# Kernel tuning notes

Measured on AMD Instinct MI355X. Metric: run time of the kernel, lower is better.

## Reference

```python
import jax, jax.numpy as jnp
import numpy as np

LEVEL = 0.1
SEED = 12345
RAND_MAX = 4294967295.0
BN_EPS = 1e-5


def lcg_noise(n):
    # Original: seed_{t+1} = (65539*seed_t + 1) & 0xFFFFFFFF; value_t = seed_{t+1}/RAND_MAX
    # Closed form: seed_{t+1} = M^{t+1} * s0 + sum_{k=0}^{t} M^k  (mod 2^32).
    # uint32 arithmetic wraps mod 2^32, so cumprod/cumsum give exact jump-ahead.
    m = jnp.full((n,), 65539, dtype=jnp.uint32)
    powers = jnp.cumprod(m)  # M^1 .. M^n (mod 2^32)
    geom = jnp.cumsum(jnp.concatenate([jnp.ones((1,), jnp.uint32), powers[:-1]]))  # sum_{k=0}^{t} M^k
    seeds = powers * jnp.uint32(SEED) + geom  # wraps mod 2^32
    return seeds.astype(jnp.float32) * jnp.float32(LEVEL / RAND_MAX)


def setup_inputs() -> dict:
    key = jax.random.key(0)
    k1, k2 = jax.random.split(key)
    B, Cin, Cout, H, W = 32, 256, 512, 64, 64
    x = jax.random.normal(k1, (B, Cin, H, W), dtype=jnp.float32)
    conv_w = jax.random.normal(k2, (Cout, Cin), dtype=jnp.float32) * 0.02
    conv_b = jnp.zeros((Cout,), dtype=jnp.float32)
    gamma = jnp.ones((Cout,), dtype=jnp.float32)
    beta = jnp.zeros((Cout,), dtype=jnp.float32)
    return {"x": x, "conv_w": conv_w, "conv_b": conv_b, "gamma": gamma, "beta": beta}


def reference(x, conv_w, conv_b, gamma, beta):
    B, C, H, W = x.shape
    noise = lcg_noise(C * H * W).reshape(C, H, W)  # batch-independent, broadcast over B
    x2 = jax.nn.relu(x + noise[None])
    # 1x1 conv == per-pixel GEMM
    y = jnp.einsum('bchw,oc->bohw', x2, conv_w) + conv_b[None, :, None, None]
    # BatchNorm2d (training mode: batch statistics, biased variance)
    mean = jnp.mean(y, axis=(0, 2, 3))
    var = jnp.var(y, axis=(0, 2, 3))
    y_hat = (y - mean[None, :, None, None]) * jax.lax.rsqrt(var + BN_EPS)[None, :, None, None]
    return y_hat * gamma[None, :, None, None] + beta[None, :, None, None]
```

## Files before the change

kernel.cpp:

```cpp
#include <hip/hip_runtime.h>
#include <cstdint>

#define B_    32
#define CIN   256
#define COUT  512
#define HW    4096
#define NPIX  (B_ * HW)
#define NOISE_N (CIN * HW)
#define WN    (COUT * CIN)

typedef _Float16 f16;
typedef _Float16 f16x8 __attribute__((ext_vector_type(8)));
typedef float    f32x4 __attribute__((ext_vector_type(4)));

__device__ __forceinline__ unsigned lcg_seed_after(unsigned n) {
  unsigned A = 1u, Bc = 0u;
  unsigned mA = 65539u, mB = 1u;
  #pragma unroll
  for (int i = 0; i < 21; ++i) {
    if (n & (1u << i)) { A = mA * A; Bc = mA * Bc + mB; }
    mB = mA * mB + mB;
    mA = mA * mA;
  }
  return A * 12345u + Bc;
}

__global__ void k_prep(const float* __restrict__ conv_w,
                       float* __restrict__ noise, f16* __restrict__ w2) {
  const int tid = blockIdx.x * 256 + threadIdx.x;
  if (tid < NOISE_N) {
    const unsigned seed = lcg_seed_after((unsigned)tid + 1u);
    noise[tid] = (float)seed * (float)(0.1 / 4294967295.0);
  } else {
    const int i = tid - NOISE_N;
    if (i < WN) w2[i] = (f16)conv_w[i];
  }
}

__global__ __launch_bounds__(1024) void k1_gram(
    const float* __restrict__ x, const float* __restrict__ noise,
    f16* __restrict__ x2t, float* __restrict__ gpart,
    float* __restrict__ sums, int npart, int useAtomic) {
  __shared__ unsigned char sm[65536];
  const int t = threadIdx.x;
  const int lane = t & 63;
  const int w = t >> 6;
  const int wm = w >> 2, wn = w & 3;
  const int bid = blockIdx.x;
  const int b = bid >> 3;
  const int hw0 = (bid & 7) << 9;

  const int pslot = t & 31;
  const int crow0 = t >> 5;

  f32x4 acc[4][4];
  #pragma unroll
  for (int i = 0; i < 4; ++i)
    #pragma unroll
    for (int j = 0; j < 4; ++j)
      acc[i][j] = (f32x4){0.f, 0.f, 0.f, 0.f};
  float csum[8] = {0.f, 0.f, 0.f, 0.f, 0.f, 0.f, 0.f, 0.f};

  for (int s = 0; s < 4; ++s) {
    const int hwS = hw0 + s * 128;
    #pragma unroll
    for (int cc = 0; cc < 8; ++cc) {
      const int c = crow0 + 32 * cc;
      const float4 xv = *(const float4*)(x + (((size_t)(b * CIN + c)) << 12) + hwS + 4 * pslot);
      const float4 nv = *(const float4*)(noise + (((size_t)c) << 12) + hwS + 4 * pslot);
      const f16 h0 = (f16)fmaxf(xv.x + nv.x, 0.f);
      const f16 h1 = (f16)fmaxf(xv.y + nv.y, 0.f);
      const f16 h2 = (f16)fmaxf(xv.z + nv.z, 0.f);
      const f16 h3 = (f16)fmaxf(xv.w + nv.w, 0.f);
      csum[cc] += (float)h0 + (float)h1 + (float)h2 + (float)h3;
      union { f16 h[2]; unsigned u; } p0, p1;
      p0.h[0] = h0; p0.h[1] = h1; p1.h[0] = h2; p1.h[1] = h3;
      const int byte = c * 256 + ((8 * pslot) ^ ((c & 7) << 4));
      *(uint2*)(sm + byte) = make_uint2(p0.u, p1.u);
    }
    __syncthreads();
    #pragma unroll
    for (int ks = 0; ks < 4; ++ks) {
      const int kb = 64 * ks + 16 * (lane >> 4);
      f16x8 af[4];
      #pragma unroll
      for (int mi = 0; mi < 4; ++mi) {
        const int c = 64 * wm + 16 * mi + (lane & 15);
        af[mi] = *(const f16x8*)(sm + c * 256 + (kb ^ ((c & 7) << 4)));
      }
      #pragma unroll
      for (int ni = 0; ni < 4; ++ni) {
        const int c2 = 64 * wn + 16 * ni + (lane & 15);
        const f16x8 bf = *(const f16x8*)(sm + c2 * 256 + (kb ^ ((c2 & 7) << 4)));
        #pragma unroll
        for (int mi = 0; mi < 4; ++mi)
          acc[mi][ni] = __builtin_amdgcn_mfma_f32_16x16x32_f16(af[mi], bf, acc[mi][ni], 0, 0, 0);
      }
    }
    {
      const int p = t & 127, cg = t >> 7;
      unsigned dw[16];
      #pragma unroll
      for (int j = 0; j < 16; ++j) {
        const int c0 = 32 * cg + 2 * j;
        const unsigned short a  = *(const unsigned short*)(sm + c0 * 256 + ((2 * p) ^ ((c0 & 7) << 4)));
        const unsigned short b2 = *(const unsigned short*)(sm + (c0 + 1) * 256 + ((2 * p) ^ (((c0 + 1) & 7) << 4)));
        dw[j] = (unsigned)a | ((unsigned)b2 << 16);
      }
      char* dst = (char*)x2t + ((size_t)(b * HW + hwS + p)) * 512 + cg * 64;
      ((uint4*)dst)[0] = make_uint4(dw[0],  dw[1],  dw[2],  dw[3]);
      ((uint4*)dst)[1] = make_uint4(dw[4],  dw[5],  dw[6],  dw[7]);
      ((uint4*)dst)[2] = make_uint4(dw[8],  dw[9],  dw[10], dw[11]);
      ((uint4*)dst)[3] = make_uint4(dw[12], dw[13], dw[14], dw[15]);
    }
    __syncthreads();
  }
  {
    float* gp = gpart + (size_t)(bid % npart) * 65536;
    if (useAtomic) {
      #pragma unroll
      for (int mi = 0; mi < 4; ++mi)
        #pragma unroll
        for (int ni = 0; ni < 4; ++ni)
          #pragma unroll
          for (int r = 0; r < 4; ++r) {
            const int m = 64 * wm + 16 * mi + 4 * (lane >> 4) + r;
            const int n = 64 * wn + 16 * ni + (lane & 15);
            atomicAdd(&gp[m * 256 + n], acc[mi][ni][r]);
          }
    } else {
      #pragma unroll
      for (int mi = 0; mi < 4; ++mi)
        #pragma unroll
        for (int ni = 0; ni < 4; ++ni)
          #pragma unroll
          for (int r = 0; r < 4; ++r) {
            const int m = 64 * wm + 16 * mi + 4 * (lane >> 4) + r;
            const int n = 64 * wn + 16 * ni + (lane & 15);
            gp[m * 256 + n] = acc[mi][ni][r];
          }
    }
  }
  {
    float* sl = (float*)sm;
    #pragma unroll
    for (int cc = 0; cc < 8; ++cc)
      sl[(crow0 + 32 * cc) * 32 + (t & 31)] = csum[cc];
    __syncthreads();
    if (t < 256) {
      float ssum = 0.f;
      #pragma unroll
      for (int i = 0; i < 32; ++i) ssum += sl[t * 32 + i];
      atomicAdd(&sums[t], ssum);
    }
  }
}

__global__ void k_greduce(const float* __restrict__ gpart, float* __restrict__ G, int npart) {
  const int i = blockIdx.x * 256 + threadIdx.x;
  float s = 0.f;
  for (int k = 0; k < npart; ++k) s += gpart[(size_t)k * 65536 + i];
  G[i] = s;
}

__global__ __launch_bounds__(256) void k_stats(
    const float* __restrict__ G, const float* __restrict__ sums,
    const f16* __restrict__ w2, const float* __restrict__ gamma,
    const float* __restrict__ beta, float* __restrict__ scale,
    float* __restrict__ shift) {
  const int o = blockIdx.x, c = threadIdx.x;
  const float wc = (float)w2[o * 256 + c];
  const float* Gr = G + c * 256;
  const f16* wr = w2 + o * 256;
  float tc = 0.f;
  for (int j = 0; j < 256; ++j) tc += Gr[j] * (float)wr[j];
  float q = wc * tc;
  float uv = wc * sums[c];
  #pragma unroll
  for (int off = 32; off > 0; off >>= 1) {
    q  += __shfl_down(q, off);
    uv += __shfl_down(uv, off);
  }
  __shared__ float rq[4], ru[4];
  const int lane = c & 63, w = c >> 6;
  if (lane == 0) { rq[w] = q; ru[w] = uv; }
  __syncthreads();
  if (c == 0) {
    const float Q = rq[0] + rq[1] + rq[2] + rq[3];
    const float U = ru[0] + ru[1] + ru[2] + ru[3];
    const float invN = 1.f / (float)NPIX;
    const float u = U * invN;
    const float var = Q * invN - u * u;
    const float sc = gamma[o] * rsqrtf(var + 1e-5f);
    scale[o] = sc;
    shift[o] = beta[o] - u * sc;
  }
}

__global__ __launch_bounds__(256) void k_gemm(
    const f16* __restrict__ w2, const f16* __restrict__ x2t,
    const float* __restrict__ scale, const float* __restrict__ shift,
    float* __restrict__ out) {
  __shared__ unsigned char sm[32768];
  const int t = threadIdx.x, lane = t & 63, w = t >> 6;
  const int wm = w >> 1, wn = w & 1;
  const int bid = blockIdx.x;
  const int ot = bid & 3;
  const int pt = bid >> 2;
  const int b = pt >> 5;
  const int hw0 = (pt & 31) << 7;
  const int o0 = ot << 7;
  const size_t gp0 = (size_t)b * HW + hw0;

  f32x4 acc[4][4];
  #pragma unroll
  for (int i = 0; i < 4; ++i)
    #pragma unroll
    for (int j = 0; j < 4; ++j)
      acc[i][j] = (f32x4){0.f, 0.f, 0.f, 0.f};

  const int r  = lane >> 3;
  const int cb = (lane & 7) << 4;
  for (int kt = 0; kt < 4; ++kt) {
    #pragma unroll
    for (int it = 0; it < 4; ++it) {
      const int idx = it * 4 + w;
      const int row = idx * 8 + r;
      const char* sa = (const char*)w2  + (size_t)(o0 + row) * 512 + kt * 128 + (cb ^ (r << 4));
      __builtin_amdgcn_global_load_lds(
          (const __attribute__((address_space(1))) void*)sa,
          (__attribute__((address_space(3))) void*)(sm + idx * 1024), 16, 0, 0);
      const char* sb = (const char*)x2t + (gp0 + row) * 512 + kt * 128 + (cb ^ (r << 4));
      __builtin_amdgcn_global_load_lds(
          (const __attribute__((address_space(1))) void*)sb,
          (__attribute__((address_space(3))) void*)(sm + 16384 + idx * 1024), 16, 0, 0);
    }
    __syncthreads();
    #pragma unroll
    for (int ks = 0; ks < 2; ++ks) {
      const int kb = 64 * ks + 16 * (lane >> 4);
      f16x8 af[4];
      #pragma unroll
      for (int mi = 0; mi < 4; ++mi) {
        const int rowa = 64 * wm + 16 * mi + (lane & 15);
        af[mi] = *(const f16x8*)(sm + rowa * 128 + (kb ^ ((rowa & 7) << 4)));
      }
      #pragma unroll
      for (int ni = 0; ni < 4; ++ni) {
        const int rowb = 64 * wn + 16 * ni + (lane & 15);
        const f16x8 bf = *(const f16x8*)(sm + 16384 + rowb * 128 + (kb ^ ((rowb & 7) << 4)));
        #pragma unroll
        for (int mi = 0; mi < 4; ++mi)
          acc[mi][ni] = __builtin_amdgcn_mfma_f32_16x16x32_f16(af[mi], bf, acc[mi][ni], 0, 0, 0);
      }
    }
    __syncthreads();
  }
  #pragma unroll
  for (int mi = 0; mi < 4; ++mi) {
    #pragma unroll
    for (int rr = 0; rr < 4; ++rr) {
      const int o = o0 + 64 * wm + 16 * mi + 4 * (lane >> 4) + rr;
      const float sc = scale[o], sh = shift[o];
      #pragma unroll
      for (int ni = 0; ni < 4; ++ni) {
        const int hw = hw0 + 64 * wn + 16 * ni + (lane & 15);
        out[(((size_t)(b * COUT + o)) << 12) + hw] = acc[mi][ni][rr] * sc + sh;
      }
    }
  }
}

extern "C" void kernel_launch(void* const* d_in, const int* in_sizes, int n_in,
                              void* d_out, int out_size, void* d_ws, size_t ws_size,
                              hipStream_t stream) {
  (void)in_sizes; (void)n_in; (void)out_size;
  const float* x      = (const float*)d_in[0];
  const float* conv_w = (const float*)d_in[1];
  const float* gamma  = (const float*)d_in[3];
  const float* beta   = (const float*)d_in[4];
  float* out = (float*)d_out;
  char* ws = (char*)d_ws;

  float* noise = (float*)(ws);
  float* G     = (float*)(ws + (4u << 20));
  f16*   w2    = (f16*)  (ws + (4u << 20) + (256u << 10));
  float* sums  = (float*)(ws + (4u << 20) + (512u << 10));
  float* scale = (float*)(ws + (4u << 20) + (514u << 10));
  float* shift = (float*)(ws + (4u << 20) + (517u << 10));
  f16*   x2t   = (f16*)  (ws + (5u << 20));
  float* gpart = (float*)(ws + (69u << 20));

  const size_t avail = ws_size > (69ull << 20) ? ws_size - (69ull << 20) : 0;
  int npart = (int)(avail / (65536ull * sizeof(float)));
  if (npart > 256) npart = 256;
  if (npart < 1) npart = 1;
  const int useAtomic = (npart < 256) ? 1 : 0;

  hipMemsetAsync(sums, 0, 256 * sizeof(float), stream);
  if (useAtomic)
    hipMemsetAsync(gpart, 0, (size_t)npart * 65536 * sizeof(float), stream);

  k_prep   <<<4608, 256,  0, stream>>>(conv_w, noise, w2);
  k1_gram  <<<256,  1024, 0, stream>>>(x, noise, x2t, gpart, sums, npart, useAtomic);
  k_greduce<<<256,  256,  0, stream>>>(gpart, G, npart);
  k_stats  <<<COUT, 256,  0, stream>>>(G, sums, w2, gamma, beta, scale, shift);
  k_gemm   <<<4096, 256,  0, stream>>>(w2, x2t, scale, shift, out);
}
```

Baseline: 550.4 us.

## Double-buffer gram and GEMM kernels, vectorize reductions, remap GEMM block order

```diff
diff --git a/kernel.cpp b/kernel.cpp
--- a/kernel.cpp
+++ b/kernel.cpp
@@ -37,11 +37,15 @@
   }
 }
 
+__device__ __forceinline__ int tadr(int c, int chunk) {
+  return (c << 6) + (((chunk ^ ((c >> 1) & 3)) & 3) << 4);
+}
+
 __global__ __launch_bounds__(1024) void k1_gram(
     const float* __restrict__ x, const float* __restrict__ noise,
     f16* __restrict__ x2t, float* __restrict__ gpart,
     float* __restrict__ sums, int npart, int useAtomic) {
-  __shared__ unsigned char sm[65536];
+  __shared__ unsigned char sm[32768];
   const int t = threadIdx.x;
   const int lane = t & 63;
   const int w = t >> 6;
@@ -50,8 +54,15 @@
   const int b = bid >> 3;
   const int hw0 = (bid & 7) << 9;
 
-  const int pslot = t & 31;
-  const int crow0 = t >> 5;
+  const int cL = t >> 2;
+  const int pq = t & 3;
+  const int p0 = pq << 3;
+  const float* xrow = x + (((size_t)(b * CIN + cL)) << 12) + hw0 + p0;
+  const float* nrow = noise + (((size_t)cL) << 12) + hw0 + p0;
+  const int wbyte = tadr(cL, pq);
+
+  const int tp = t & 31;
+  const int c0 = (t >> 5) << 3;
 
   f32x4 acc[4][4];
   #pragma unroll
@@ -59,62 +70,76 @@
     #pragma unroll
     for (int j = 0; j < 4; ++j)
       acc[i][j] = (f32x4){0.f, 0.f, 0.f, 0.f};
-  float csum[8] = {0.f, 0.f, 0.f, 0.f, 0.f, 0.f, 0.f, 0.f};
-
-  for (int s = 0; s < 4; ++s) {
-    const int hwS = hw0 + s * 128;
-    #pragma unroll
-    for (int cc = 0; cc < 8; ++cc) {
-      const int c = crow0 + 32 * cc;
-      const float4 xv = *(const float4*)(x + (((size_t)(b * CIN + c)) << 12) + hwS + 4 * pslot);
-      const float4 nv = *(const float4*)(noise + (((size_t)c) << 12) + hwS + 4 * pslot);
-      const f16 h0 = (f16)fmaxf(xv.x + nv.x, 0.f);
-      const f16 h1 = (f16)fmaxf(xv.y + nv.y, 0.f);
-      const f16 h2 = (f16)fmaxf(xv.z + nv.z, 0.f);
-      const f16 h3 = (f16)fmaxf(xv.w + nv.w, 0.f);
-      csum[cc] += (float)h0 + (float)h1 + (float)h2 + (float)h3;
-      union { f16 h[2]; unsigned u; } p0, p1;
-      p0.h[0] = h0; p0.h[1] = h1; p1.h[0] = h2; p1.h[1] = h3;
-      const int byte = c * 256 + ((8 * pslot) ^ ((c & 7) << 4));
-      *(uint2*)(sm + byte) = make_uint2(p0.u, p1.u);
-    }
-    __syncthreads();
-    #pragma unroll
-    for (int ks = 0; ks < 4; ++ks) {
-      const int kb = 64 * ks + 16 * (lane >> 4);
+  float csum = 0.f;
+
+  {
+    const float4 xa = *(const float4*)(xrow);
+    const float4 xb = *(const float4*)(xrow + 4);
+    const float4 na = *(const float4*)(nrow);
+    const float4 nb = *(const float4*)(nrow + 4);
+    f16x8 hv;
+    hv[0] = (f16)fmaxf(xa.x + na.x, 0.f); hv[1] = (f16)fmaxf(xa.y + na.y, 0.f);
+    hv[2] = (f16)fmaxf(xa.z + na.z, 0.f); hv[3] = (f16)fmaxf(xa.w + na.w, 0.f);
+    hv[4] = (f16)fmaxf(xb.x + nb.x, 0.f); hv[5] = (f16)fmaxf(xb.y + nb.y, 0.f);
+    hv[6] = (f16)fmaxf(xb.z + nb.z, 0.f); hv[7] = (f16)fmaxf(xb.w + nb.w, 0.f);
+    #pragma unroll
+    for (int i = 0; i < 8; ++i) csum += (float)hv[i];
+    *(f16x8*)(sm + wbyte) = hv;
+  }
+  __syncthreads();
+
+  for (int s = 0; s < 16; ++s) {
+    const int base = (s & 1) << 14;
+    float4 xa, xb;
+    if (s < 15) {
+      xa = *(const float4*)(xrow + (s + 1) * 32);
+      xb = *(const float4*)(xrow + (s + 1) * 32 + 4);
+    }
+    {
+      const int ch = lane >> 4;
       f16x8 af[4];
       #pragma unroll
-      for (int mi = 0; mi < 4; ++mi) {
-        const int c = 64 * wm + 16 * mi + (lane & 15);
-        af[mi] = *(const f16x8*)(sm + c * 256 + (kb ^ ((c & 7) << 4)));
-      }
+      for (int mi = 0; mi < 4; ++mi)
+        af[mi] = *(const f16x8*)(sm + base + tadr(wm * 64 + mi * 16 + (lane & 15), ch));
       #pragma unroll
       for (int ni = 0; ni < 4; ++ni) {
-        const int c2 = 64 * wn + 16 * ni + (lane & 15);
-        const f16x8 bf = *(const f16x8*)(sm + c2 * 256 + (kb ^ ((c2 & 7) << 4)));
+        const f16x8 bf = *(const f16x8*)(sm + base + tadr(wn * 64 + ni * 16 + (lane & 15), ch));
         #pragma unroll
         for (int mi = 0; mi < 4; ++mi)
           acc[mi][ni] = __builtin_amdgcn_mfma_f32_16x16x32_f16(af[mi], bf, acc[mi][ni], 0, 0, 0);
       }
     }
+    uint4 pk;
     {
-      const int p = t & 127, cg = t >> 7;
-      unsigned dw[16];
-      #pragma unroll
-      for (int j = 0; j < 16; ++j) {
-        const int c0 = 32 * cg + 2 * j;
-        const unsigned short a  = *(const unsigned short*)(sm + c0 * 256 + ((2 * p) ^ ((c0 & 7) << 4)));
-        const unsigned short b2 = *(const unsigned short*)(sm + (c0 + 1) * 256 + ((2 * p) ^ (((c0 + 1) & 7) << 4)));
-        dw[j] = (unsigned)a | ((unsigned)b2 << 16);
-      }
-      char* dst = (char*)x2t + ((size_t)(b * HW + hwS + p)) * 512 + cg * 64;
-      ((uint4*)dst)[0] = make_uint4(dw[0],  dw[1],  dw[2],  dw[3]);
-      ((uint4*)dst)[1] = make_uint4(dw[4],  dw[5],  dw[6],  dw[7]);
-      ((uint4*)dst)[2] = make_uint4(dw[8],  dw[9],  dw[10], dw[11]);
-      ((uint4*)dst)[3] = make_uint4(dw[12], dw[13], dw[14], dw[15]);
+      unsigned short vals[8];
+      #pragma unroll
+      for (int j = 0; j < 8; ++j) {
+        const int row = c0 + j;
+        const int addr = base + (row << 6) + ((2 * tp) & 15) +
+                         ((((tp >> 3) ^ ((row >> 1) & 3)) & 3) << 4);
+        vals[j] = *(const unsigned short*)(sm + addr);
+      }
+      pk.x = (unsigned)vals[0] | ((unsigned)vals[1] << 16);
+      pk.y = (unsigned)vals[2] | ((unsigned)vals[3] << 16);
+      pk.z = (unsigned)vals[4] | ((unsigned)vals[5] << 16);
+      pk.w = (unsigned)vals[6] | ((unsigned)vals[7] << 16);
+    }
+    if (s < 15) {
+      const float4 na = *(const float4*)(nrow + (s + 1) * 32);
+      const float4 nb = *(const float4*)(nrow + (s + 1) * 32 + 4);
+      f16x8 hv;
+      hv[0] = (f16)fmaxf(xa.x + na.x, 0.f); hv[1] = (f16)fmaxf(xa.y + na.y, 0.f);
+      hv[2] = (f16)fmaxf(xa.z + na.z, 0.f); hv[3] = (f16)fmaxf(xa.w + na.w, 0.f);
+      hv[4] = (f16)fmaxf(xb.x + nb.x, 0.f); hv[5] = (f16)fmaxf(xb.y + nb.y, 0.f);
+      hv[6] = (f16)fmaxf(xb.z + nb.z, 0.f); hv[7] = (f16)fmaxf(xb.w + nb.w, 0.f);
+      #pragma unroll
+      for (int i = 0; i < 8; ++i) csum += (float)hv[i];
+      *(f16x8*)(sm + (base ^ 16384) + wbyte) = hv;
     }
     __syncthreads();
-  }
+    *(uint4*)((char*)x2t + ((size_t)(b * HW + hw0 + s * 32 + tp)) * 512 + (c0 << 1)) = pk;
+  }
+
   {
     float* gp = gpart + (size_t)(bid % npart) * 65536;
     if (useAtomic) {
@@ -143,24 +168,27 @@
   }
   {
     float* sl = (float*)sm;
-    #pragma unroll
-    for (int cc = 0; cc < 8; ++cc)
-      sl[(crow0 + 32 * cc) * 32 + (t & 31)] = csum[cc];
+    sl[(cL << 2) + pq] = csum;
     __syncthreads();
     if (t < 256) {
-      float ssum = 0.f;
-      #pragma unroll
-      for (int i = 0; i < 32; ++i) ssum += sl[t * 32 + i];
-      atomicAdd(&sums[t], ssum);
+      const float* r4 = sl + (t << 2);
+      atomicAdd(&sums[t], (r4[0] + r4[1]) + (r4[2] + r4[3]));
     }
   }
 }
 
 __global__ void k_greduce(const float* __restrict__ gpart, float* __restrict__ G, int npart) {
   const int i = blockIdx.x * 256 + threadIdx.x;
-  float s = 0.f;
-  for (int k = 0; k < npart; ++k) s += gpart[(size_t)k * 65536 + i];
-  G[i] = s;
+  float s0 = 0.f, s1 = 0.f, s2 = 0.f, s3 = 0.f;
+  int k = 0;
+  for (; k + 4 <= npart; k += 4) {
+    s0 += gpart[(size_t)(k + 0) * 65536 + i];
+    s1 += gpart[(size_t)(k + 1) * 65536 + i];
+    s2 += gpart[(size_t)(k + 2) * 65536 + i];
+    s3 += gpart[(size_t)(k + 3) * 65536 + i];
+  }
+  for (; k < npart; ++k) s0 += gpart[(size_t)k * 65536 + i];
+  G[i] = (s0 + s1) + (s2 + s3);
 }
 
 __global__ __launch_bounds__(256) void k_stats(
@@ -170,10 +198,16 @@
     float* __restrict__ shift) {
   const int o = blockIdx.x, c = threadIdx.x;
   const float wc = (float)w2[o * 256 + c];
-  const float* Gr = G + c * 256;
+  const float4* G4 = (const float4*)(G + (c << 8));
   const f16* wr = w2 + o * 256;
   float tc = 0.f;
-  for (int j = 0; j < 256; ++j) tc += Gr[j] * (float)wr[j];
+  #pragma unroll 4
+  for (int j8 = 0; j8 < 32; ++j8) {
+    const f16x8 wv = *(const f16x8*)(wr + j8 * 8);
+    const float4 ga = G4[2 * j8], gb = G4[2 * j8 + 1];
+    tc += ga.x * (float)wv[0] + ga.y * (float)wv[1] + ga.z * (float)wv[2] + ga.w * (float)wv[3]
+        + gb.x * (float)wv[4] + gb.y * (float)wv[5] + gb.z * (float)wv[6] + gb.w * (float)wv[7];
+  }
   float q = wc * tc;
   float uv = wc * sums[c];
   #pragma unroll
@@ -201,10 +235,10 @@
     const f16* __restrict__ w2, const f16* __restrict__ x2t,
     const float* __restrict__ scale, const float* __restrict__ shift,
     float* __restrict__ out) {
-  __shared__ unsigned char sm[32768];
+  __shared__ unsigned char sm[65536];
   const int t = threadIdx.x, lane = t & 63, w = t >> 6;
   const int wm = w >> 1, wn = w & 1;
-  const int bid = blockIdx.x;
+  const int bid = (blockIdx.x & 7) * 512 + (blockIdx.x >> 3);
   const int ot = bid & 3;
   const int pt = bid >> 2;
   const int b = pt >> 5;
@@ -221,21 +255,31 @@
 
   const int r  = lane >> 3;
   const int cb = (lane & 7) << 4;
+  const int cbs = cb ^ (r << 4);
+
+  #define STAGE(kt, buf)                                                          \
+    {                                                                             \
+      const int bb = (buf) << 15;                                                 \
+      _Pragma("unroll")                                                           \
+      for (int it = 0; it < 4; ++it) {                                            \
+        const int idx = it * 4 + w;                                               \
+        const int row = idx * 8 + r;                                              \
+        const char* sa = (const char*)w2 + (size_t)(o0 + row) * 512 + (kt) * 128 + cbs; \
+        __builtin_amdgcn_global_load_lds(                                         \
+            (const __attribute__((address_space(1))) void*)sa,                    \
+            (__attribute__((address_space(3))) void*)(sm + bb + idx * 1024), 16, 0, 0); \
+        const char* sb = (const char*)x2t + (gp0 + row) * 512 + (kt) * 128 + cbs; \
+        __builtin_amdgcn_global_load_lds(                                         \
+            (const __attribute__((address_space(1))) void*)sb,                    \
+            (__attribute__((address_space(3))) void*)(sm + bb + 16384 + idx * 1024), 16, 0, 0); \
+      }                                                                           \
+    }
+
+  STAGE(0, 0);
+  __syncthreads();
   for (int kt = 0; kt < 4; ++kt) {
-    #pragma unroll
-    for (int it = 0; it < 4; ++it) {
-      const int idx = it * 4 + w;
-      const int row = idx * 8 + r;
-      const char* sa = (const char*)w2  + (size_t)(o0 + row) * 512 + kt * 128 + (cb ^ (r << 4));
-      __builtin_amdgcn_global_load_lds(
-          (const __attribute__((address_space(1))) void*)sa,
-          (__attribute__((address_space(3))) void*)(sm + idx * 1024), 16, 0, 0);
-      const char* sb = (const char*)x2t + (gp0 + row) * 512 + kt * 128 + (cb ^ (r << 4));
-      __builtin_amdgcn_global_load_lds(
-          (const __attribute__((address_space(1))) void*)sb,
-          (__attribute__((address_space(3))) void*)(sm + 16384 + idx * 1024), 16, 0, 0);
-    }
-    __syncthreads();
+    if (kt < 3) STAGE(kt + 1, (kt + 1) & 1);
+    const int base = (kt & 1) << 15;
     #pragma unroll
     for (int ks = 0; ks < 2; ++ks) {
       const int kb = 64 * ks + 16 * (lane >> 4);
@@ -243,12 +287,12 @@
       #pragma unroll
       for (int mi = 0; mi < 4; ++mi) {
         const int rowa = 64 * wm + 16 * mi + (lane & 15);
-        af[mi] = *(const f16x8*)(sm + rowa * 128 + (kb ^ ((rowa & 7) << 4)));
+        af[mi] = *(const f16x8*)(sm + base + rowa * 128 + (kb ^ ((rowa & 7) << 4)));
       }
       #pragma unroll
       for (int ni = 0; ni < 4; ++ni) {
         const int rowb = 64 * wn + 16 * ni + (lane & 15);
-        const f16x8 bf = *(const f16x8*)(sm + 16384 + rowb * 128 + (kb ^ ((rowb & 7) << 4)));
+        const f16x8 bf = *(const f16x8*)(sm + base + 16384 + rowb * 128 + (kb ^ ((rowb & 7) << 4)));
         #pragma unroll
         for (int mi = 0; mi < 4; ++mi)
           acc[mi][ni] = __builtin_amdgcn_mfma_f32_16x16x32_f16(af[mi], bf, acc[mi][ni], 0, 0, 0);
@@ -256,6 +300,8 @@
     }
     __syncthreads();
   }
+  #undef STAGE
+
   #pragma unroll
   for (int mi = 0; mi < 4; ++mi) {
     #pragma unroll
```

Result: faster. 491.8 us (-10.6%).
